# Kernel tuning notes

Measured on AMD Instinct MI355X. Metric: run time of the kernel, lower is better.

Reference implementation:

```python
import jax, jax.numpy as jnp
import numpy as np

B, N, F, DM, DMO, OM, L = 32, 64, 64, 128, 64, 128, 4
PRE_H, PRE_O, POST_H = 128, 64, 64
E = N * N
EPS = 1e-5


def swish(x):
    return x * jax.nn.sigmoid(x)


def bn_edges(x, g, b):
    # BatchNorm1d(num_features=E) applied to [B, E, D]: per-edge-channel stats over (batch, D)
    m = x.mean(axis=(0, 2), keepdims=True)
    v = x.var(axis=(0, 2), keepdims=True)
    return (x - m) / jnp.sqrt(v + EPS) * g[None, :, None] + b[None, :, None]


def setup_inputs():
    key = jax.random.key(0)
    ks = iter(jax.random.split(key, 64))

    def rn(shape, s=0.05):
        return jax.random.normal(next(ks), shape, dtype=jnp.float32) * s

    # fully-connected graph incl. self-loops (required by BatchNorm1d(n_nodes^2))
    src, dst = np.meshgrid(np.arange(N), np.arange(N), indexing='ij')
    edge_index = jnp.asarray(np.stack([src.reshape(-1), dst.reshape(-1)]), dtype=jnp.int32)
    return {
        'node_feature': rn((B, N, F), 1.0),
        'vectors': rn((B, N, OM), 1.0),
        'edge_index': edge_index,
        'msg_W1': rn((L, 2 * F, DM)), 'msg_b1': rn((L, DM)),
        'bn1_g': jnp.ones((L, E), jnp.float32), 'bn1_b': jnp.zeros((L, E), jnp.float32),
        'msg_W2': rn((L, DM, DM)), 'msg_b2': rn((L, DM)),
        'bn2_g': jnp.ones((L, E), jnp.float32), 'bn2_b': jnp.zeros((L, E), jnp.float32),
        'msg_W3': rn((L, DM, DM)), 'msg_b3': rn((L, DM)),
        'bn3_g': jnp.ones((L, E), jnp.float32), 'bn3_b': jnp.zeros((L, E), jnp.float32),
        'msg_W4': rn((L, DM, DMO)), 'msg_b4': rn((L, DMO)),
        'upd_W1': rn((L, OM + F + DMO, DM)), 'upd_b1': rn((L, DM)),
        'upd_W2': rn((L, DM, DM)), 'upd_b2': rn((L, DM)),
        'upd_W3': rn((L, DM, DM)), 'upd_b3': rn((L, DM)),
        'upd_W4': rn((L, DM, F)), 'upd_b4': rn((L, F)),
        'pre_W1': rn((F, PRE_H)), 'pre_b1': rn((PRE_H,)),
        'pre_W2': rn((PRE_H, PRE_H)), 'pre_b2': rn((PRE_H,)),
        'pre_W3': rn((PRE_H, PRE_H)), 'pre_b3': rn((PRE_H,)),
        'pre_W4': rn((PRE_H, PRE_O)), 'pre_b4': rn((PRE_O,)),
        'post_W1': rn((PRE_O, POST_H)), 'post_b1': rn((POST_H,)),
        'post_W2': rn((POST_H, 1)), 'post_b2': rn((1,)),
    }


def reference(node_feature, vectors, edge_index,
              msg_W1, msg_b1, bn1_g, bn1_b, msg_W2, msg_b2, bn2_g, bn2_b,
              msg_W3, msg_b3, bn3_g, bn3_b, msg_W4, msg_b4,
              upd_W1, upd_b1, upd_W2, upd_b2, upd_W3, upd_b3, upd_W4, upd_b4,
              pre_W1, pre_b1, pre_W2, pre_b2, pre_W3, pre_b3, pre_W4, pre_b4,
              post_W1, post_b1, post_W2, post_b2):
    src, dst = edge_index[0], edge_index[1]
    x = node_feature  # [B, N, F]
    v = vectors       # [B, N, OM]
    cnt = jax.ops.segment_sum(jnp.ones((E,), jnp.float32), dst, num_segments=N)
    inv_cnt = 1.0 / jnp.maximum(cnt, 1.0)
    for l in range(L):
        x_i = x[:, dst]  # [B, E, F] gather targets
        x_j = x[:, src]  # [B, E, F] gather sources
        h = swish(jnp.concatenate([x_i, x_j], -1) @ msg_W1[l] + msg_b1[l])
        h = bn_edges(h, bn1_g[l], bn1_b[l])
        h = bn_edges(swish(h @ msg_W2[l] + msg_b2[l]), bn2_g[l], bn2_b[l])
        h = bn_edges(swish(h @ msg_W3[l] + msg_b3[l]), bn3_g[l], bn3_b[l])
        m = swish(h @ msg_W4[l] + msg_b4[l])  # [B, E, DMO]
        agg = jax.ops.segment_sum(jnp.transpose(m, (1, 0, 2)), dst, num_segments=N)
        agg = jnp.transpose(agg, (1, 0, 2)) * inv_cnt[None, :, None]  # mean aggr, [B, N, DMO]
        u = jnp.concatenate([v, x, agg], -1)  # [B, N, OM+F+DMO]
        h = swish(u @ upd_W1[l] + upd_b1[l])
        h = swish(h @ upd_W2[l] + upd_b2[l])
        h = swish(h @ upd_W3[l] + upd_b3[l])
        x = x + swish(h @ upd_W4[l] + upd_b4[l])  # residual update
    h = swish(x @ pre_W1 + pre_b1)
    h = swish(h @ pre_W2 + pre_b2)
    h = swish(h @ pre_W3 + pre_b3)
    h = h @ pre_W4 + pre_b4
    c = swish(h @ post_W1 + post_b1) @ post_W2 + post_b2  # [B, N, 1]
    x3 = jnp.einsum('bnd,bn->bd', v, c[..., 0])           # coefficient-weighted vector sum
    return x3, v, c
```

## Files before the change

### kernel.cpp

```cpp
#include <hip/hip_runtime.h>
#include <hip/hip_bf16.h>

typedef unsigned short u16t;
typedef __attribute__((ext_vector_type(8))) short bf16x8;
typedef __attribute__((ext_vector_type(4))) short bf16x4;
typedef __attribute__((ext_vector_type(4))) float f32x4;

#define Bn 32
#define Nn 64
#define Fd 64
#define DMd 128
#define DMOd 64
#define OMd 128
#define En 4096

#define NTEN 36
#define TOTALC 1073217
#define HP 136
#define UP 264
#define XP 72
#define WSEG 131072

__device__ const int kOffs[NTEN + 1] = {
    0,        131072,   393216,   458752,   459264,   475648,   492032,   557568,
    558080,   574464,   590848,   656384,   656896,   673280,   689664,   722432,
    722688,   853760,   854272,   919808,   920320,   985856,   986368,   1019136,
    1019392,  1027584,  1027712,  1044096,  1044224,  1060608,  1060736,  1068928,
    1068992,  1073088,  1073152,  1073216,  1073217
};

#define C_NF    0
#define C_VEC   131072
#define C_MW1   393216
#define C_MB1   458752
#define C_G1    459264
#define C_BB1   475648
#define C_MW2   492032
#define C_MB2   557568
#define C_G2    558080
#define C_BB2   574464
#define C_MW3   590848
#define C_MB3   656384
#define C_G3    656896
#define C_BB3   673280
#define C_MW4   689664
#define C_MB4   722432
#define C_UW1   722688
#define C_UB1   853760
#define C_UW2   854272
#define C_UB2   919808
#define C_UW3   920320
#define C_UB3   985856
#define C_UW4   986368
#define C_UB4   1019136
#define C_PW1   1019392
#define C_PB1   1027584
#define C_PW2   1027712
#define C_PB2   1044096
#define C_PW3   1044224
#define C_PB3   1060608
#define C_PW4   1060736
#define C_PB4   1068928
#define C_QW1   1068992
#define C_QB1   1073088
#define C_QW2   1073152
#define C_QB2   1073216

#define S_W2T 0
#define S_W3T 16384
#define S_W4T 32768
#define S_U1T 40960
#define S_U2T 73728
#define S_U3T 90112
#define S_U4T 106496
#define S_W1T 114688

#define NB_CONV 4193
#define NB_PREPW 2048
#define NB_CS 5
#define NB_PQ0 1024
#define NB_PREP (NB_CONV + NB_PREPW + NB_CS + NB_PQ0)

struct Ptrs { const void* p[NTEN]; };

__device__ __forceinline__ float us2f(u16t u) {
    return __uint_as_float(((unsigned int)u) << 16);
}
__device__ __forceinline__ u16t f2us(float f) {
    __hip_bfloat16 h = __float2bfloat16(f);
    return *reinterpret_cast<u16t*>(&h);
}
__device__ __forceinline__ float swishf(float x) {
    return x * __builtin_amdgcn_rcpf(1.0f + __expf(-x));
}
__device__ __forceinline__ float ldcvt(const void* p, int idx, int flag) {
    return flag ? us2f(((const u16t*)p)[idx]) : ((const float*)p)[idx];
}
__device__ __forceinline__ int get_flag(const void* g1raw) {
    return (((const u16t*)g1raw)[0] == 0x3F80u) ? 1 : 0;
}

__global__ __launch_bounds__(256) void k_prep(Ptrs t, float* __restrict__ C,
                                              float* __restrict__ x,
                                              u16t* __restrict__ W,
                                              float* __restrict__ CS,
                                              float* __restrict__ P,
                                              float* __restrict__ Q,
                                              float* __restrict__ agg) {
    const int flag = get_flag(t.p[4]);
    const int blk = blockIdx.x;
    const int tid = threadIdx.x;

    if (blk < NB_CONV) {
        int i = blk * 256 + tid;
        if (i >= TOTALC) return;
        int lo = 0, hi = NTEN;
        while (hi - lo > 1) { int m = (lo + hi) >> 1; if (i >= kOffs[m]) lo = m; else hi = m; }
        const int local = i - kOffs[lo];
        float v = ldcvt(t.p[lo], local, flag);
        C[i] = v;
        if (i < Bn * Nn * Fd) x[i] = v;
    } else if (blk < NB_CONV + NB_PREPW) {
        int i = (blk - NB_CONV) * 256 + tid;
        const int l = i / WSEG;
        int r = i - l * WSEG;
        int tens, local;
        if (r < S_W3T)      { int q = r;          int n = q >> 7, k = q & 127; tens = 6;  local = l*16384 + k*128 + n; }
        else if (r < S_W4T) { int q = r - S_W3T;  int n = q >> 7, k = q & 127; tens = 10; local = l*16384 + k*128 + n; }
        else if (r < S_U1T) { int q = r - S_W4T;  int n = q >> 7, k = q & 127; tens = 14; local = l*8192  + k*64  + n; }
        else if (r < S_U2T) { int q = r - S_U1T;  int n = q >> 8, k = q & 255; tens = 16; local = l*32768 + k*128 + n; }
        else if (r < S_U3T) { int q = r - S_U2T;  int n = q >> 7, k = q & 127; tens = 18; local = l*16384 + k*128 + n; }
        else if (r < S_U4T) { int q = r - S_U3T;  int n = q >> 7, k = q & 127; tens = 20; local = l*16384 + k*128 + n; }
        else if (r < S_W1T) { int q = r - S_U4T;  int n = q >> 7, k = q & 127; tens = 22; local = l*8192  + k*64  + n; }
        else                { int q = r - S_W1T;  int n = q >> 7, k = q & 127; tens = 2;  local = l*16384 + k*128 + n; }
        W[i] = f2us(ldcvt(t.p[tens], local, flag));
    } else if (blk < NB_CONV + NB_PREPW + NB_CS) {
        int i = (blk - NB_CONV - NB_PREPW) * 256 + tid;
        if (i >= 4 * 320) return;
        const int l = i / 320, j = i - l * 320;
        const void* tp; int base, stride;
        if (j < 128)      { tp = t.p[6];  base = l*16384 + j;         stride = 128; }
        else if (j < 256) { tp = t.p[10]; base = l*16384 + (j - 128); stride = 128; }
        else              { tp = t.p[14]; base = l*8192  + (j - 256); stride = 64; }
        float s = 0.f;
        #pragma unroll 8
        for (int k = 0; k < 128; k++) s += us2f(f2us(ldcvt(tp, base + k * stride, flag)));
        CS[i] = s;
    } else {
        const int rel = blk - (NB_CONV + NB_PREPW + NB_CS);
        const int gid = rel * 256 + tid;
        if (gid < Bn * Nn * DMOd) agg[gid] = 0.f;
        __shared__ float xr2[2][Fd];
        const int half = tid >> 7, t7 = tid & 127;
        const int bn = rel * 2 + half;
        if (t7 < Fd) xr2[half][t7] = ldcvt(t.p[0], bn * Fd + t7, flag);
        __syncthreads();
        float accP = 0.f, accQ = 0.f;
        if (flag) {
            const u16t* W1 = (const u16t*)t.p[2];
            #pragma unroll 8
            for (int k = 0; k < Fd; k++) {
                float xv = xr2[half][k];
                accP += xv * us2f(W1[k * DMd + t7]);
                accQ += xv * us2f(W1[(Fd + k) * DMd + t7]);
            }
        } else {
            const float* W1 = (const float*)t.p[2];
            #pragma unroll 8
            for (int k = 0; k < Fd; k++) {
                float xv = xr2[half][k];
                accP += xv * W1[k * DMd + t7];
                accQ += xv * W1[(Fd + k) * DMd + t7];
            }
        }
        P[bn * DMd + t7] = accP;
        Q[bn * DMd + t7] = accQ;
    }
}

__device__ __forceinline__ void wave_red8(float* s, float (*rd)[8], int wv, int lane) {
    #pragma unroll
    for (int off = 32; off > 0; off >>= 1)
        #pragma unroll
        for (int k = 0; k < 8; k++) s[k] += __shfl_down(s[k], off);
    if (lane == 0) {
        #pragma unroll
        for (int k = 0; k < 8; k++) rd[wv][k] = s[k];
    }
}

__device__ __forceinline__ void calc_ab(const float (*rd)[8],
                                        const float* __restrict__ g,
                                        const float* __restrict__ bb,
                                        int src0, int dst,
                                        float* a, float* c) {
    #pragma unroll
    for (int e = 0; e < 4; e++) {
        float S  = rd[0][2*e]   + rd[1][2*e]   + rd[2][2*e]   + rd[3][2*e];
        float S2 = rd[0][2*e+1] + rd[1][2*e+1] + rd[2][2*e+1] + rd[3][2*e+1];
        float mean = S * (1.0f / 4096.0f);
        float var  = S2 * (1.0f / 4096.0f) - mean * mean;
        float av = rsqrtf(var + 1e-5f) * g[(src0 + e) * Nn + dst];
        a[e] = av;
        c[e] = bb[(src0 + e) * Nn + dst] - mean * av;
    }
}

__global__ __launch_bounds__(256, 4) void k_edge(
    const float* __restrict__ P, const float* __restrict__ Q,
    const float* __restrict__ b1v,
    const float* __restrict__ g1, const float* __restrict__ bb1,
    const u16t* __restrict__ W2t, const float* __restrict__ b2v, const float* __restrict__ cs2,
    const float* __restrict__ g2, const float* __restrict__ bb2,
    const u16t* __restrict__ W3t, const float* __restrict__ b3v, const float* __restrict__ cs3,
    const float* __restrict__ g3, const float* __restrict__ bb3,
    const u16t* __restrict__ W4t, const float* __restrict__ b4v, const float* __restrict__ cs4,
    float* __restrict__ agg) {
    __shared__ u16t hE[4][Bn * HP];
    __shared__ float red[2][4][8];

    const int dst = blockIdx.x & 63, src0 = (blockIdx.x >> 6) * 4;
    const int tid = threadIdx.x;
    const int wv = tid >> 6, lane = tid & 63, quad = lane >> 4, l15 = lane & 15;
    const int mw = wv & 1, nb2 = wv >> 1;
    const int mrow = mw * 16 + l15;
    const int nBase = nb2 * 64;

    {
        const int b = tid >> 3, d0 = (tid & 7) * 16;
        float4 pv[4], bv4[4];
        {
            const float4* pp = (const float4*)&P[(b * Nn + dst) * DMd + d0];
            const float4* bp = (const float4*)&b1v[d0];
            #pragma unroll
            for (int j = 0; j < 4; j++) { pv[j] = pp[j]; bv4[j] = bp[j]; }
        }
        float s[8];
        #pragma unroll
        for (int e = 0; e < 4; e++) {
            const float4* qq = (const float4*)&Q[(b * Nn + src0 + e) * DMd + d0];
            float u[16];
            #pragma unroll
            for (int j = 0; j < 4; j++) {
                float4 qv = qq[j];
                u[j*4+0] = swishf(pv[j].x + qv.x + bv4[j].x);
                u[j*4+1] = swishf(pv[j].y + qv.y + bv4[j].y);
                u[j*4+2] = swishf(pv[j].z + qv.z + bv4[j].z);
                u[j*4+3] = swishf(pv[j].w + qv.w + bv4[j].w);
            }
            float se = 0.f, s2e = 0.f;
            #pragma unroll
            for (int i = 0; i < 16; i++) { se += u[i]; s2e += u[i] * u[i]; }
            bf16x8 s0, s1;
            #pragma unroll
            for (int j = 0; j < 8; j++) {
                s0[j] = (short)f2us(u[j]);
                s1[j] = (short)f2us(u[8 + j]);
            }
            *(bf16x8*)&hE[e][b * HP + d0]     = s0;
            *(bf16x8*)&hE[e][b * HP + d0 + 8] = s1;
            s[2*e] = se; s[2*e+1] = s2e;
        }
        wave_red8(s, red[0], wv, lane);
    }
    __syncthreads();

    float aP[4], cP[4];
    calc_ab(red[0], g1, bb1, src0, dst, aP, cP);

    #pragma unroll 1
    for (int st = 0; st < 2; st++) {
        const u16t*  Wt = st ? W3t : W2t;
        const float* bv = st ? b3v : b2v;
        const float* cv = st ? cs3 : cs2;
        bf16x4 pk[4][4];
        float s[8];
        #pragma unroll
        for (int eh = 0; eh < 2; eh++) {
            f32x4 acc[2][4];
            #pragma unroll
            for (int ee = 0; ee < 2; ee++)
                #pragma unroll
                for (int t = 0; t < 4; t++) acc[ee][t] = (f32x4){0.f, 0.f, 0.f, 0.f};
            #pragma unroll
            for (int ks = 0; ks < 4; ks++) {
                bf16x8 wb[4];
                #pragma unroll
                for (int t = 0; t < 4; t++)
                    wb[t] = *(const bf16x8*)&Wt[(nBase + t * 16 + l15) * 128 + ks * 32 + quad * 8];
                #pragma unroll
                for (int ee = 0; ee < 2; ee++) {
                    bf16x8 a8 = *(const bf16x8*)&hE[eh * 2 + ee][mrow * HP + ks * 32 + quad * 8];
                    #pragma unroll
                    for (int t = 0; t < 4; t++)
                        acc[ee][t] = __builtin_amdgcn_mfma_f32_16x16x32_bf16(wb[t], a8, acc[ee][t], 0, 0, 0);
                }
            }
            #pragma unroll
            for (int ee = 0; ee < 2; ee++) {
                const int e = eh * 2 + ee;
                const float ae = aP[e], ce = cP[e];
                float se = 0.f, s2e = 0.f;
                #pragma unroll
                for (int t = 0; t < 4; t++) {
                    const int n0 = nBase + t * 16 + quad * 4;
                    float4 c4  = *(const float4*)&cv[n0];
                    float4 bb4 = *(const float4*)&bv[n0];
                    #pragma unroll
                    for (int r = 0; r < 4; r++) {
                        float z = ae * acc[ee][t][r] + (ce * (&c4.x)[r] + (&bb4.x)[r]);
                        float u = swishf(z);
                        se += u; s2e += u * u;
                        pk[e][t][r] = (short)f2us(u);
                    }
                }
                s[2*e] = se; s[2*e+1] = s2e;
            }
        }
        wave_red8(s, red[1 - st], wv, lane);
        __syncthreads();
        calc_ab(red[1 - st], st ? g3 : g2, st ? bb3 : bb2, src0, dst, aP, cP);
        #pragma unroll
        for (int e = 0; e < 4; e++)
            #pragma unroll
            for (int t = 0; t < 4; t++)
                *(bf16x4*)&hE[e][mrow * HP + nBase + t * 16 + quad * 4] = pk[e][t];
        __syncthreads();
    }

    {
        const int n40 = nb2 * 32;
        f32x4 a4[4][2];
        #pragma unroll
        for (int e = 0; e < 4; e++) {
            a4[e][0] = (f32x4){0.f, 0.f, 0.f, 0.f};
            a4[e][1] = (f32x4){0.f, 0.f, 0.f, 0.f};
        }
        #pragma unroll
        for (int ks = 0; ks < 4; ks++) {
            bf16x8 wb[2];
            #pragma unroll
            for (int t = 0; t < 2; t++)
                wb[t] = *(const bf16x8*)&W4t[(n40 + t * 16 + l15) * 128 + ks * 32 + quad * 8];
            #pragma unroll
            for (int e = 0; e < 4; e++) {
                bf16x8 a8 = *(const bf16x8*)&hE[e][mrow * HP + ks * 32 + quad * 8];
                #pragma unroll
                for (int t = 0; t < 2; t++)
                    a4[e][t] = __builtin_amdgcn_mfma_f32_16x16x32_bf16(a8, wb[t], a4[e][t], 0, 0, 0);
            }
        }
        #pragma unroll
        for (int t = 0; t < 2; t++) {
            const int col = n40 + t * 16 + l15;
            const float csv = cs4[col], bvv = b4v[col];
            float fe[4];
            #pragma unroll
            for (int e = 0; e < 4; e++) fe[e] = cP[e] * csv + bvv;
            #pragma unroll
            for (int r = 0; r < 4; r++) {
                float m = swishf(aP[0] * a4[0][t][r] + fe[0])
                        + swishf(aP[1] * a4[1][t][r] + fe[1])
                        + swishf(aP[2] * a4[2][t][r] + fe[2])
                        + swishf(aP[3] * a4[3][t][r] + fe[3]);
                const int b = mw * 16 + quad * 4 + r;
                atomicAdd(&agg[(b * Nn + dst) * DMOd + col], m);
            }
        }
    }
}

__global__ __launch_bounds__(256, 4) void k_updq(
    const float* __restrict__ vC, float* __restrict__ x, float* __restrict__ agg,
    const u16t* __restrict__ U1t, const float* __restrict__ b1,
    const u16t* __restrict__ U2t, const float* __restrict__ b2,
    const u16t* __restrict__ U3t, const float* __restrict__ b3,
    const u16t* __restrict__ U4t, const float* __restrict__ b4,
    const u16t* __restrict__ W1Tn, float* __restrict__ Pn, float* __restrict__ Qn,
    int doPQ) {
    __shared__ u16t uL[16 * UP];
    __shared__ u16t hL[16 * HP];
    __shared__ u16t xL[16 * XP];
    const int g0 = blockIdx.x * 16;
    const int tid = threadIdx.x;
    const int wv = tid >> 6, lane = tid & 63, quad = lane >> 4, l15 = lane & 15;
    const int nBase = wv * 32;

    {
        const int i = tid >> 4, c0 = (tid & 15) * 16;
        const int g = g0 + i;
        const float* srcp; float scl = 1.f;
        if (c0 < 128)       srcp = &vC[g * OMd + c0];
        else if (c0 < 192)  srcp = &x[g * Fd + (c0 - 128)];
        else              { srcp = &agg[g * DMOd + (c0 - 192)]; scl = 1.0f / 64.0f; }
        bf16x8 s0, s1;
        #pragma unroll
        for (int j = 0; j < 8; j++) {
            s0[j] = (short)f2us(srcp[j] * scl);
            s1[j] = (short)f2us(srcp[8 + j] * scl);
        }
        *(bf16x8*)&uL[i * UP + c0]     = s0;
        *(bf16x8*)&uL[i * UP + c0 + 8] = s1;
    }
    __syncthreads();

    {
        f32x4 acc[2];
        #pragma unroll
        for (int t = 0; t < 2; t++) {
            float b0 = b1[nBase + t * 16 + l15];
            acc[t] = (f32x4){b0, b0, b0, b0};
        }
        #pragma unroll
        for (int ks = 0; ks < 8; ks++) {
            bf16x8 a8 = *(const bf16x8*)&uL[l15 * UP + ks * 32 + quad * 8];
            #pragma unroll
            for (int t = 0; t < 2; t++) {
                bf16x8 b8 = *(const bf16x8*)&U1t[(nBase + t * 16 + l15) * 256 + ks * 32 + quad * 8];
                acc[t] = __builtin_amdgcn_mfma_f32_16x16x32_bf16(a8, b8, acc[t], 0, 0, 0);
            }
        }
        #pragma unroll
        for (int t = 0; t < 2; t++)
            #pragma unroll
            for (int r = 0; r < 4; r++)
                hL[(quad * 4 + r) * HP + nBase + t * 16 + l15] = f2us(swishf(acc[t][r]));
    }
    __syncthreads();

    #pragma unroll 1
    for (int st = 0; st < 2; st++) {
        const u16t*  Ut = st ? U3t : U2t;
        const float* bb = st ? b3  : b2;
        f32x4 acc[2];
        #pragma unroll
        for (int t = 0; t < 2; t++) {
            float b0 = bb[nBase + t * 16 + l15];
            acc[t] = (f32x4){b0, b0, b0, b0};
        }
        #pragma unroll
        for (int ks = 0; ks < 4; ks++) {
            bf16x8 a8 = *(const bf16x8*)&hL[l15 * HP + ks * 32 + quad * 8];
            #pragma unroll
            for (int t = 0; t < 2; t++) {
                bf16x8 b8 = *(const bf16x8*)&Ut[(nBase + t * 16 + l15) * 128 + ks * 32 + quad * 8];
                acc[t] = __builtin_amdgcn_mfma_f32_16x16x32_bf16(a8, b8, acc[t], 0, 0, 0);
            }
        }
        __syncthreads();
        #pragma unroll
        for (int t = 0; t < 2; t++)
            #pragma unroll
            for (int r = 0; r < 4; r++)
                hL[(quad * 4 + r) * HP + nBase + t * 16 + l15] = f2us(swishf(acc[t][r]));
        __syncthreads();
    }

    {
        const int n4 = wv * 16;
        f32x4 acc;
        {
            float b0 = b4[n4 + l15];
            acc = (f32x4){b0, b0, b0, b0};
        }
        #pragma unroll
        for (int ks = 0; ks < 4; ks++) {
            bf16x8 a8 = *(const bf16x8*)&hL[l15 * HP + ks * 32 + quad * 8];
            bf16x8 b8 = *(const bf16x8*)&U4t[(n4 + l15) * 128 + ks * 32 + quad * 8];
            acc = __builtin_amdgcn_mfma_f32_16x16x32_bf16(a8, b8, acc, 0, 0, 0);
        }
        #pragma unroll
        for (int r = 0; r < 4; r++) {
            int row = quad * 4 + r, col = n4 + l15;
            float xn = x[(g0 + row) * Fd + col] + swishf(acc[r]);
            x[(g0 + row) * Fd + col] = xn;
            xL[row * XP + col] = f2us(xn);
        }
    }

    {
        int idx = tid;
        #pragma unroll
        for (int k = 0; k < 4; k++, idx += 256) agg[g0 * DMOd + idx] = 0.f;
    }
    __syncthreads();

    if (doPQ) {
        f32x4 ap[2], aq[2];
        #pragma unroll
        for (int j = 0; j < 2; j++) { ap[j] = (f32x4){0,0,0,0}; aq[j] = (f32x4){0,0,0,0}; }
        #pragma unroll
        for (int ks = 0; ks < 2; ks++) {
            bf16x8 a8 = *(const bf16x8*)&xL[l15 * XP + ks * 32 + quad * 8];
            #pragma unroll
            for (int j = 0; j < 2; j++) {
                const int n0 = (wv * 2 + j) * 16 + l15;
                bf16x8 bp = *(const bf16x8*)&W1Tn[n0 * 128 + ks * 32 + quad * 8];
                bf16x8 bq = *(const bf16x8*)&W1Tn[n0 * 128 + 64 + ks * 32 + quad * 8];
                ap[j] = __builtin_amdgcn_mfma_f32_16x16x32_bf16(a8, bp, ap[j], 0, 0, 0);
                aq[j] = __builtin_amdgcn_mfma_f32_16x16x32_bf16(a8, bq, aq[j], 0, 0, 0);
            }
        }
        #pragma unroll
        for (int j = 0; j < 2; j++)
            #pragma unroll
            for (int r = 0; r < 4; r++) {
                int g = g0 + quad * 4 + r, col = (wv * 2 + j) * 16 + l15;
                Pn[g * DMd + col] = ap[j][r];
                Qn[g * DMd + col] = aq[j][r];
            }
    }
}

__global__ __launch_bounds__(128) void k_final(
    const float* __restrict__ x, const void* __restrict__ vraw,
    const float* __restrict__ pW1, const float* __restrict__ pb1,
    const float* __restrict__ pW2, const float* __restrict__ pb2,
    const float* __restrict__ pW3, const float* __restrict__ pb3,
    const float* __restrict__ pW4, const float* __restrict__ pb4,
    const float* __restrict__ qW1, const float* __restrict__ qb1,
    const float* __restrict__ qW2, const float* __restrict__ qb2,
    float* __restrict__ c_buf, void* __restrict__ out, const void* __restrict__ g1raw) {
    __shared__ float xr[64];
    __shared__ float ha[128];
    __shared__ float hb[128];
    __shared__ float hc[64];
    __shared__ float tt[64];
    const int bn = blockIdx.x;
    const int tid = threadIdx.x;
    const int flag = get_flag(g1raw);
    if (tid < 64) xr[tid] = x[bn * Fd + tid];
    __syncthreads();
    float acc = pb1[tid];
    #pragma unroll 8
    for (int k = 0; k < 64; k++) acc += xr[k] * pW1[k * 128 + tid];
    ha[tid] = swishf(acc);
    __syncthreads();
    acc = pb2[tid];
    #pragma unroll 8
    for (int k = 0; k < 128; k++) acc += ha[k] * pW2[k * 128 + tid];
    hb[tid] = swishf(acc);
    __syncthreads();
    acc = pb3[tid];
    #pragma unroll 8
    for (int k = 0; k < 128; k++) acc += hb[k] * pW3[k * 128 + tid];
    ha[tid] = swishf(acc);
    __syncthreads();
    if (tid < 64) {
        acc = pb4[tid];
        #pragma unroll 8
        for (int k = 0; k < 128; k++) acc += ha[k] * pW4[k * 64 + tid];
        hc[tid] = acc;
    }
    __syncthreads();
    if (tid < 64) {
        acc = qb1[tid];
        #pragma unroll 8
        for (int k = 0; k < 64; k++) acc += hc[k] * qW1[k * 64 + tid];
        tt[tid] = swishf(acc);
    }
    __syncthreads();
    if (tid < 64) {
        float p = tt[tid] * qW2[tid];
        #pragma unroll
        for (int off = 32; off > 0; off >>= 1) p += __shfl_down(p, off);
        if (tid == 0) {
            float cv = p + qb2[0];
            c_buf[bn] = cv;
            const int ci = 4096 + Bn * Nn * OMd + bn;
            if (flag) ((u16t*)out)[ci] = f2us(cv);
            else      ((float*)out)[ci] = cv;
        }
    }
    const int vi = bn * OMd + tid;
    if (flag) ((u16t*)out)[4096 + vi] = ((const u16t*)vraw)[vi];
    else      ((float*)out)[4096 + vi] = ((const float*)vraw)[vi];
}

__global__ __launch_bounds__(128) void k_x3(const float* __restrict__ vC,
                                            const float* __restrict__ c_buf,
                                            void* __restrict__ out,
                                            const void* __restrict__ g1raw) {
    const int b = blockIdx.x, d = threadIdx.x;
    const int flag = get_flag(g1raw);
    float acc = 0.f;
    #pragma unroll 4
    for (int n = 0; n < Nn; n++)
        acc += vC[(b * Nn + n) * OMd + d] * c_buf[b * Nn + n];
    if (flag) ((u16t*)out)[b * OMd + d] = f2us(acc);
    else      ((float*)out)[b * OMd + d] = acc;
}

extern "C" void kernel_launch(void* const* d_in, const int* in_sizes, int n_in,
                              void* d_out, int out_size, void* d_ws, size_t ws_size,
                              hipStream_t stream) {
    float* ws = (float*)d_ws;
    float* C     = ws + 16;
    float* x     = C + 1073664;
    float* P     = x + 131072;
    float* Q     = P + 262144;
    float* agg   = Q + 262144;
    float* c_buf = agg + 131072;
    u16t*  Wt    = (u16t*)(c_buf + 2048);
    float* CS    = (float*)(Wt + 4 * WSEG);

    Ptrs t;
    for (int i = 0, j = 0; i < 37; i++) {
        if (i == 2) continue;
        t.p[j++] = d_in[i];
    }

    k_prep<<<NB_PREP, 256, 0, stream>>>(t, C, x, Wt, CS, P, Q, agg);

    for (int l = 0; l < 4; l++) {
        u16t* Wl = Wt + l * WSEG;
        float* CSl = CS + l * 320;
        k_edge<<<64 * 16, 256, 0, stream>>>(
            P, Q,
            C + C_MB1 + l * DMd, C + C_G1 + l * En, C + C_BB1 + l * En,
            Wl + S_W2T, C + C_MB2 + l * DMd, CSl,
            C + C_G2 + l * En, C + C_BB2 + l * En,
            Wl + S_W3T, C + C_MB3 + l * DMd, CSl + 128,
            C + C_G3 + l * En, C + C_BB3 + l * En,
            Wl + S_W4T, C + C_MB4 + l * DMOd, CSl + 256,
            agg);
        const int doPQ = (l < 3) ? 1 : 0;
        const u16t* W1Tn = Wt + (doPQ ? (l + 1) : 0) * WSEG + S_W1T;
        k_updq<<<Bn * Nn / 16, 256, 0, stream>>>(
            C + C_VEC, x, agg,
            Wl + S_U1T, C + C_UB1 + l * DMd,
            Wl + S_U2T, C + C_UB2 + l * DMd,
            Wl + S_U3T, C + C_UB3 + l * DMd,
            Wl + S_U4T, C + C_UB4 + l * DMOd,
            W1Tn, P, Q, doPQ);
    }

    k_final<<<Bn * Nn, 128, 0, stream>>>(x, d_in[1],
        C + C_PW1, C + C_PB1, C + C_PW2, C + C_PB2,
        C + C_PW3, C + C_PB3, C + C_PW4, C + C_PB4,
        C + C_QW1, C + C_QB1, C + C_QW2, C + C_QB2,
        c_buf, d_out, d_in[5]);
    k_x3<<<Bn, 128, 0, stream>>>(C + C_VEC, c_buf, d_out, d_in[5]);
}
```

Measured before the change: 386.3 us.

## Assign one edge per wave in k_edge to remove block-wide BN reductions

```diff
diff --git a/kernel.cpp b/kernel.cpp
--- a/kernel.cpp
+++ b/kernel.cpp
@@ -178,35 +178,7 @@
     }
 }
 
-__device__ __forceinline__ void wave_red8(float* s, float (*rd)[8], int wv, int lane) {
-    #pragma unroll
-    for (int off = 32; off > 0; off >>= 1)
-        #pragma unroll
-        for (int k = 0; k < 8; k++) s[k] += __shfl_down(s[k], off);
-    if (lane == 0) {
-        #pragma unroll
-        for (int k = 0; k < 8; k++) rd[wv][k] = s[k];
-    }
-}
-
-__device__ __forceinline__ void calc_ab(const float (*rd)[8],
-                                        const float* __restrict__ g,
-                                        const float* __restrict__ bb,
-                                        int src0, int dst,
-                                        float* a, float* c) {
-    #pragma unroll
-    for (int e = 0; e < 4; e++) {
-        float S  = rd[0][2*e]   + rd[1][2*e]   + rd[2][2*e]   + rd[3][2*e];
-        float S2 = rd[0][2*e+1] + rd[1][2*e+1] + rd[2][2*e+1] + rd[3][2*e+1];
-        float mean = S * (1.0f / 4096.0f);
-        float var  = S2 * (1.0f / 4096.0f) - mean * mean;
-        float av = rsqrtf(var + 1e-5f) * g[(src0 + e) * Nn + dst];
-        a[e] = av;
-        c[e] = bb[(src0 + e) * Nn + dst] - mean * av;
-    }
-}
-
-__global__ __launch_bounds__(256, 4) void k_edge(
+__global__ __launch_bounds__(256, 3) void k_edge(
     const float* __restrict__ P, const float* __restrict__ Q,
     const float* __restrict__ b1v,
     const float* __restrict__ g1, const float* __restrict__ bb1,
@@ -217,155 +189,149 @@
     const u16t* __restrict__ W4t, const float* __restrict__ b4v, const float* __restrict__ cs4,
     float* __restrict__ agg) {
     __shared__ u16t hE[4][Bn * HP];
-    __shared__ float red[2][4][8];
 
     const int dst = blockIdx.x & 63, src0 = (blockIdx.x >> 6) * 4;
     const int tid = threadIdx.x;
     const int wv = tid >> 6, lane = tid & 63, quad = lane >> 4, l15 = lane & 15;
-    const int mw = wv & 1, nb2 = wv >> 1;
-    const int mrow = mw * 16 + l15;
-    const int nBase = nb2 * 64;
-
-    {
-        const int b = tid >> 3, d0 = (tid & 7) * 16;
-        float4 pv[4], bv4[4];
-        {
-            const float4* pp = (const float4*)&P[(b * Nn + dst) * DMd + d0];
-            const float4* bp = (const float4*)&b1v[d0];
-            #pragma unroll
-            for (int j = 0; j < 4; j++) { pv[j] = pp[j]; bv4[j] = bp[j]; }
-        }
-        float s[8];
-        #pragma unroll
-        for (int e = 0; e < 4; e++) {
-            const float4* qq = (const float4*)&Q[(b * Nn + src0 + e) * DMd + d0];
-            float u[16];
-            #pragma unroll
-            for (int j = 0; j < 4; j++) {
-                float4 qv = qq[j];
-                u[j*4+0] = swishf(pv[j].x + qv.x + bv4[j].x);
-                u[j*4+1] = swishf(pv[j].y + qv.y + bv4[j].y);
-                u[j*4+2] = swishf(pv[j].z + qv.z + bv4[j].z);
-                u[j*4+3] = swishf(pv[j].w + qv.w + bv4[j].w);
-            }
-            float se = 0.f, s2e = 0.f;
-            #pragma unroll
-            for (int i = 0; i < 16; i++) { se += u[i]; s2e += u[i] * u[i]; }
-            bf16x8 s0, s1;
-            #pragma unroll
-            for (int j = 0; j < 8; j++) {
-                s0[j] = (short)f2us(u[j]);
-                s1[j] = (short)f2us(u[8 + j]);
-            }
-            *(bf16x8*)&hE[e][b * HP + d0]     = s0;
-            *(bf16x8*)&hE[e][b * HP + d0 + 8] = s1;
-            s[2*e] = se; s[2*e+1] = s2e;
-        }
-        wave_red8(s, red[0], wv, lane);
-    }
-    __syncthreads();
-
-    float aP[4], cP[4];
-    calc_ab(red[0], g1, bb1, src0, dst, aP, cP);
+    const int src = src0 + wv;
+    u16t* hme = hE[wv];
+
+    float se = 0.f, s2e = 0.f;
+    {
+        const int b = lane & 31, d0 = (lane >> 5) * 64;
+        const float4* pp = (const float4*)&P[(b * Nn + dst) * DMd + d0];
+        const float4* qq = (const float4*)&Q[(b * Nn + src) * DMd + d0];
+        const float4* bp = (const float4*)&b1v[d0];
+        #pragma unroll
+        for (int j = 0; j < 8; j++) {
+            float4 p0 = pp[2*j], p1 = pp[2*j+1];
+            float4 q0 = qq[2*j], q1 = qq[2*j+1];
+            float4 c0 = bp[2*j], c1 = bp[2*j+1];
+            float u[8];
+            u[0] = swishf(p0.x + q0.x + c0.x); u[1] = swishf(p0.y + q0.y + c0.y);
+            u[2] = swishf(p0.z + q0.z + c0.z); u[3] = swishf(p0.w + q0.w + c0.w);
+            u[4] = swishf(p1.x + q1.x + c1.x); u[5] = swishf(p1.y + q1.y + c1.y);
+            u[6] = swishf(p1.z + q1.z + c1.z); u[7] = swishf(p1.w + q1.w + c1.w);
+            bf16x8 pk;
+            #pragma unroll
+            for (int i = 0; i < 8; i++) {
+                se += u[i]; s2e += u[i] * u[i];
+                pk[i] = (short)f2us(u[i]);
+            }
+            *(bf16x8*)&hme[b * HP + d0 + j * 8] = pk;
+        }
+    }
+    #pragma unroll
+    for (int off = 32; off; off >>= 1) { se += __shfl_xor(se, off); s2e += __shfl_xor(s2e, off); }
+    float aP, cP;
+    {
+        float mean = se * (1.0f / 4096.0f);
+        float var  = s2e * (1.0f / 4096.0f) - mean * mean;
+        aP = rsqrtf(var + 1e-5f) * g1[src * Nn + dst];
+        cP = bb1[src * Nn + dst] - mean * aP;
+    }
 
     #pragma unroll 1
     for (int st = 0; st < 2; st++) {
         const u16t*  Wt = st ? W3t : W2t;
         const float* bv = st ? b3v : b2v;
         const float* cv = st ? cs3 : cs2;
-        bf16x4 pk[4][4];
-        float s[8];
-        #pragma unroll
-        for (int eh = 0; eh < 2; eh++) {
-            f32x4 acc[2][4];
-            #pragma unroll
-            for (int ee = 0; ee < 2; ee++)
+        f32x4 acc[2][8];
+        #pragma unroll
+        for (int mt = 0; mt < 2; mt++)
+            #pragma unroll
+            for (int nt = 0; nt < 8; nt++) acc[mt][nt] = (f32x4){0.f, 0.f, 0.f, 0.f};
+        #pragma unroll
+        for (int ks = 0; ks < 4; ks++) {
+            bf16x8 a80 = *(const bf16x8*)&hme[l15 * HP + ks * 32 + quad * 8];
+            bf16x8 a81 = *(const bf16x8*)&hme[(16 + l15) * HP + ks * 32 + quad * 8];
+            #pragma unroll
+            for (int nt = 0; nt < 8; nt++) {
+                bf16x8 wb = *(const bf16x8*)&Wt[(nt * 16 + l15) * 128 + ks * 32 + quad * 8];
+                acc[0][nt] = __builtin_amdgcn_mfma_f32_16x16x32_bf16(wb, a80, acc[0][nt], 0, 0, 0);
+                acc[1][nt] = __builtin_amdgcn_mfma_f32_16x16x32_bf16(wb, a81, acc[1][nt], 0, 0, 0);
+            }
+        }
+        float seN = 0.f, s2N = 0.f;
+        #pragma unroll
+        for (int mt = 0; mt < 2; mt++)
+            #pragma unroll
+            for (int nt = 0; nt < 8; nt++) {
+                const int n0 = nt * 16 + quad * 4;
+                float4 c4  = *(const float4*)&cv[n0];
+                float4 bb4 = *(const float4*)&bv[n0];
                 #pragma unroll
-                for (int t = 0; t < 4; t++) acc[ee][t] = (f32x4){0.f, 0.f, 0.f, 0.f};
-            #pragma unroll
-            for (int ks = 0; ks < 4; ks++) {
-                bf16x8 wb[4];
+                for (int r = 0; r < 4; r++) {
+                    float z = aP * acc[mt][nt][r] + (cP * (&c4.x)[r] + (&bb4.x)[r]);
+                    float u = swishf(z);
+                    acc[mt][nt][r] = u;
+                    seN += u; s2N += u * u;
+                }
+            }
+        #pragma unroll
+        for (int off = 32; off; off >>= 1) { seN += __shfl_xor(seN, off); s2N += __shfl_xor(s2N, off); }
+        {
+            float mean = seN * (1.0f / 4096.0f);
+            float var  = s2N * (1.0f / 4096.0f) - mean * mean;
+            const float* gv  = st ? g3  : g2;
+            const float* bbv = st ? bb3 : bb2;
+            aP = rsqrtf(var + 1e-5f) * gv[src * Nn + dst];
+            cP = bbv[src * Nn + dst] - mean * aP;
+        }
+        #pragma unroll
+        for (int mt = 0; mt < 2; mt++)
+            #pragma unroll
+            for (int nt = 0; nt < 8; nt++) {
+                bf16x4 pk;
                 #pragma unroll
-                for (int t = 0; t < 4; t++)
-                    wb[t] = *(const bf16x8*)&Wt[(nBase + t * 16 + l15) * 128 + ks * 32 + quad * 8];
+                for (int r = 0; r < 4; r++) pk[r] = (short)f2us(acc[mt][nt][r]);
+                *(bf16x4*)&hme[(mt * 16 + l15) * HP + nt * 16 + quad * 4] = pk;
+            }
+    }
+
+    {
+        f32x4 a4[2][4];
+        #pragma unroll
+        for (int mt = 0; mt < 2; mt++)
+            #pragma unroll
+            for (int nt = 0; nt < 4; nt++) a4[mt][nt] = (f32x4){0.f, 0.f, 0.f, 0.f};
+        #pragma unroll
+        for (int ks = 0; ks < 4; ks++) {
+            bf16x8 a80 = *(const bf16x8*)&hme[l15 * HP + ks * 32 + quad * 8];
+            bf16x8 a81 = *(const bf16x8*)&hme[(16 + l15) * HP + ks * 32 + quad * 8];
+            #pragma unroll
+            for (int nt = 0; nt < 4; nt++) {
+                bf16x8 wb = *(const bf16x8*)&W4t[(nt * 16 + l15) * 128 + ks * 32 + quad * 8];
+                a4[0][nt] = __builtin_amdgcn_mfma_f32_16x16x32_bf16(wb, a80, a4[0][nt], 0, 0, 0);
+                a4[1][nt] = __builtin_amdgcn_mfma_f32_16x16x32_bf16(wb, a81, a4[1][nt], 0, 0, 0);
+            }
+        }
+        float* mf = (float*)&hE[wv][0];
+        #pragma unroll
+        for (int mt = 0; mt < 2; mt++)
+            #pragma unroll
+            for (int nt = 0; nt < 4; nt++) {
+                const int n0 = nt * 16 + quad * 4;
+                float4 c4  = *(const float4*)&cs4[n0];
+                float4 bb4 = *(const float4*)&b4v[n0];
+                f32x4 mv;
                 #pragma unroll
-                for (int ee = 0; ee < 2; ee++) {
-                    bf16x8 a8 = *(const bf16x8*)&hE[eh * 2 + ee][mrow * HP + ks * 32 + quad * 8];
-                    #pragma unroll
-                    for (int t = 0; t < 4; t++)
-                        acc[ee][t] = __builtin_amdgcn_mfma_f32_16x16x32_bf16(wb[t], a8, acc[ee][t], 0, 0, 0);
-                }
-            }
-            #pragma unroll
-            for (int ee = 0; ee < 2; ee++) {
-                const int e = eh * 2 + ee;
-                const float ae = aP[e], ce = cP[e];
-                float se = 0.f, s2e = 0.f;
-                #pragma unroll
-                for (int t = 0; t < 4; t++) {
-                    const int n0 = nBase + t * 16 + quad * 4;
-                    float4 c4  = *(const float4*)&cv[n0];
-                    float4 bb4 = *(const float4*)&bv[n0];
-                    #pragma unroll
-                    for (int r = 0; r < 4; r++) {
-                        float z = ae * acc[ee][t][r] + (ce * (&c4.x)[r] + (&bb4.x)[r]);
-                        float u = swishf(z);
-                        se += u; s2e += u * u;
-                        pk[e][t][r] = (short)f2us(u);
-                    }
-                }
-                s[2*e] = se; s[2*e+1] = s2e;
-            }
-        }
-        wave_red8(s, red[1 - st], wv, lane);
-        __syncthreads();
-        calc_ab(red[1 - st], st ? g3 : g2, st ? bb3 : bb2, src0, dst, aP, cP);
-        #pragma unroll
-        for (int e = 0; e < 4; e++)
-            #pragma unroll
-            for (int t = 0; t < 4; t++)
-                *(bf16x4*)&hE[e][mrow * HP + nBase + t * 16 + quad * 4] = pk[e][t];
-        __syncthreads();
-    }
-
-    {
-        const int n40 = nb2 * 32;
-        f32x4 a4[4][2];
-        #pragma unroll
-        for (int e = 0; e < 4; e++) {
-            a4[e][0] = (f32x4){0.f, 0.f, 0.f, 0.f};
-            a4[e][1] = (f32x4){0.f, 0.f, 0.f, 0.f};
-        }
-        #pragma unroll
-        for (int ks = 0; ks < 4; ks++) {
-            bf16x8 wb[2];
-            #pragma unroll
-            for (int t = 0; t < 2; t++)
-                wb[t] = *(const bf16x8*)&W4t[(n40 + t * 16 + l15) * 128 + ks * 32 + quad * 8];
-            #pragma unroll
-            for (int e = 0; e < 4; e++) {
-                bf16x8 a8 = *(const bf16x8*)&hE[e][mrow * HP + ks * 32 + quad * 8];
-                #pragma unroll
-                for (int t = 0; t < 2; t++)
-                    a4[e][t] = __builtin_amdgcn_mfma_f32_16x16x32_bf16(a8, wb[t], a4[e][t], 0, 0, 0);
-            }
-        }
-        #pragma unroll
-        for (int t = 0; t < 2; t++) {
-            const int col = n40 + t * 16 + l15;
-            const float csv = cs4[col], bvv = b4v[col];
-            float fe[4];
-            #pragma unroll
-            for (int e = 0; e < 4; e++) fe[e] = cP[e] * csv + bvv;
-            #pragma unroll
-            for (int r = 0; r < 4; r++) {
-                float m = swishf(aP[0] * a4[0][t][r] + fe[0])
-                        + swishf(aP[1] * a4[1][t][r] + fe[1])
-                        + swishf(aP[2] * a4[2][t][r] + fe[2])
-                        + swishf(aP[3] * a4[3][t][r] + fe[3]);
-                const int b = mw * 16 + quad * 4 + r;
-                atomicAdd(&agg[(b * Nn + dst) * DMOd + col], m);
-            }
+                for (int r = 0; r < 4; r++)
+                    mv[r] = swishf(aP * a4[mt][nt][r] + (cP * (&c4.x)[r] + (&bb4.x)[r]));
+                *(f32x4*)&mf[(mt * 16 + l15) * 68 + n0] = mv;
+            }
+    }
+    __syncthreads();
+
+    {
+        const float* mfall = (const float*)hE;
+        #pragma unroll
+        for (int j = 0; j < 8; j++) {
+            const int idx = j * 256 + tid;
+            const int row = idx >> 6, col = idx & 63;
+            const int li = row * 68 + col;
+            float v = mfall[li] + mfall[2176 + li] + mfall[2 * 2176 + li] + mfall[3 * 2176 + li];
+            atomicAdd(&agg[(row * Nn + dst) * DMOd + col], v);
         }
     }
 }
```

Result: slower. 538.7 us (+39.4%).
